# Kernel optimization log

Hardware: AMD Instinct MI355X
Metric: run time of the kernel (lower is better)

The kernel has to match this reference:

```python
import jax, jax.numpy as jnp
import numpy as np

N_NODES = 100000
N_EDGES = 2000000
FEAT = 4
H = 64
L = 3  # num_mp_layers
E = 2  # edge_types


def _p(key, shape, scale=0.05):
    return jax.random.normal(key, shape, dtype=jnp.float32) * scale


def setup_inputs() -> dict:
    key = jax.random.key(0)
    ks = jax.random.split(key, 24)
    inp = {
        "x": jax.random.normal(ks[0], (N_NODES, FEAT), dtype=jnp.float32),
        "node_type": jax.random.randint(ks[1], (N_NODES,), 0, 3),
        "edge_index": jax.random.randint(ks[2], (2, N_EDGES), 0, N_NODES),
        "edge_type": jax.random.randint(ks[3], (N_EDGES,), 0, E),
        # input_proj: Linear(4,64) + LayerNorm(64)
        "in_w": _p(ks[4], (FEAT, H)), "in_b": _p(ks[5], (H,)),
        "ln_g": jnp.ones((H,), jnp.float32), "ln_b": jnp.zeros((H,), jnp.float32),
        # per-layer, per-edge-type message MLPs: Linear(2H,H) -> ReLU -> Linear(H,H)
        "mlp_w1": _p(ks[6], (L, E, 2 * H, H)), "mlp_b1": _p(ks[7], (L, E, H)),
        "mlp_w2": _p(ks[8], (L, E, H, H)), "mlp_b2": _p(ks[9], (L, E, H)),
        # per-layer GRUCell(H,H): gates ordered [r, z, n] as in torch
        "gru_wi": _p(ks[10], (L, H, 3 * H)), "gru_wh": _p(ks[11], (L, H, 3 * H)),
        "gru_bi": _p(ks[12], (L, 3 * H)), "gru_bh": _p(ks[13], (L, 3 * H)),
        # readout: Linear(H,H) -> ReLU -> Linear(H,1)
        "ro_w1": _p(ks[14], (H, H)), "ro_b1": _p(ks[15], (H,)),
        "ro_w2": _p(ks[16], (H, 1)), "ro_b2": _p(ks[17], (1,)),
    }
    return inp


def _layernorm(h, g, b, eps=1e-5):
    mu = jnp.mean(h, axis=-1, keepdims=True)
    var = jnp.mean(jnp.square(h - mu), axis=-1, keepdims=True)
    return (h - mu) * jax.lax.rsqrt(var + eps) * g + b


def _forward(x, edge_index, edge_type, node_type,
             in_w, in_b, ln_g, ln_b,
             mlp_w1, mlp_b1, mlp_w2, mlp_b2,
             gru_wi, gru_wh, gru_bi, gru_bh,
             ro_w1, ro_b1, ro_w2, ro_b2):
    n = x.shape[0]
    # input projection (dropout is identity at inference)
    h = jax.nn.relu(_layernorm(x @ in_w + in_b, ln_g, ln_b))
    src, dst = edge_index[0], edge_index[1]
    for l in range(L):
        # gather -> concat: (M, 2H)
        mi = jnp.concatenate([h[src], h[dst]], axis=1)
        msg = jnp.zeros((mi.shape[0], H), dtype=h.dtype)
        for e in range(E):
            m = jax.nn.relu(mi @ mlp_w1[l, e] + mlp_b1[l, e]) @ mlp_w2[l, e] + mlp_b2[l, e]
            msg = msg + jnp.where((edge_type == e)[:, None], m, jnp.zeros((), h.dtype))
        # scatter_add over destination nodes
        agg = jax.ops.segment_sum(msg, dst, num_segments=n)
        # GRUCell(agg, h), torch gate order [r, z, n]
        gi = agg @ gru_wi[l] + gru_bi[l]
        gh = h @ gru_wh[l] + gru_bh[l]
        i_r, i_z, i_n = jnp.split(gi, 3, axis=-1)
        h_r, h_z, h_n = jnp.split(gh, 3, axis=-1)
        r = jax.nn.sigmoid(i_r + h_r)
        z = jax.nn.sigmoid(i_z + h_z)
        nn_ = jnp.tanh(i_n + r * h_n)
        h = (1.0 - z) * nn_ + z * h
    out = jax.nn.relu(h @ ro_w1 + ro_b1) @ ro_w2 + ro_b2  # (N, 1)
    # additive correction for data qubits (node_type==0); other nodes zeroed
    corr = jnp.where(node_type == 0, x[:, 0] + out[:, 0], jnp.zeros((), x.dtype))
    return corr


def reference(x, node_type, edge_index, edge_type,
              in_w, in_b, ln_g, ln_b,
              mlp_w1, mlp_b1, mlp_w2, mlp_b2,
              gru_wi, gru_wh, gru_bi, gru_bh,
              ro_w1, ro_b1, ro_w2, ro_b2):
    return _forward(x, edge_index, edge_type, node_type,
                    in_w, in_b, ln_g, ln_b,
                    mlp_w1, mlp_b1, mlp_w2, mlp_b2,
                    gru_wi, gru_wh, gru_bi, gru_bh,
                    ro_w1, ro_b1, ro_w2, ro_b2)
```

## Files before the change

### kernel.cpp

```cpp
#include <hip/hip_runtime.h>

typedef unsigned int u32;
typedef unsigned short u16;
typedef unsigned long long u64;

using short8 = __attribute__((ext_vector_type(8))) short;
using f32x4  = __attribute__((ext_vector_type(4))) float;

__device__ __forceinline__ u32 f2bf(float f) {
    u32 u = __float_as_uint(f);
    return (u + 0x7fffu + ((u >> 16) & 1u)) >> 16;
}
__device__ __forceinline__ u32 pk(float a, float b) {
    return f2bf(a) | (f2bf(b) << 16);
}
__device__ __forceinline__ u32 f2bf_fast(float f) {
    return (__float_as_uint(f) + 0x8000u) >> 16;
}
__device__ __forceinline__ u32 pk_fast(float a, float b) {
    return f2bf_fast(a) | (f2bf_fast(b) << 16);
}
__device__ __forceinline__ float bflo(u32 u) { return __uint_as_float(u << 16); }
__device__ __forceinline__ float bfhi(u32 u) { return __uint_as_float(u & 0xffff0000u); }
__device__ __forceinline__ float bfu(u16 u) { return __uint_as_float(((u32)u) << 16); }

union U8 { u32 u[4]; short8 v; };

__global__ void k_input_proj(const float* __restrict__ x, const float* __restrict__ in_w,
                             const float* __restrict__ in_b, const float* __restrict__ ln_g,
                             const float* __restrict__ ln_b, u16* __restrict__ hbf,
                             float* __restrict__ agg, int n_nodes) {
    const int lane = threadIdx.x & 63;
    const int node = blockIdx.x * 4 + (threadIdx.x >> 6);
    if (node >= n_nodes) return;
    agg[(size_t)node * 64 + lane] = 0.f;
    float acc = in_b[lane];
#pragma unroll
    for (int k = 0; k < 4; ++k) acc = fmaf(x[node * 4 + k], in_w[k * 64 + lane], acc);
    float s = acc;
#pragma unroll
    for (int off = 32; off > 0; off >>= 1) s += __shfl_xor(s, off);
    float mu = s * (1.f / 64.f);
    float d = acc - mu;
    float vs = d * d;
#pragma unroll
    for (int off = 32; off > 0; off >>= 1) vs += __shfl_xor(vs, off);
    float inv = rsqrtf(vs * (1.f / 64.f) + 1e-5f);
    float hv = fmaxf(d * inv * ln_g[lane] + ln_b[lane], 0.f);
    hbf[(size_t)node * 64 + lane] = (u16)f2bf(hv);
}

__global__ void k_hist(const int* __restrict__ dst, const int* __restrict__ ety,
                       int* __restrict__ cnt, int* __restrict__ key, int M, int N) {
    int i = blockIdx.x * 256 + threadIdx.x;
    if (i < M) {
        int k = (ety[i] & 1) * N + dst[i];
        key[i] = k;
        atomicAdd(&cnt[k], 1);
    }
}

__global__ void k_scan1(int* __restrict__ data, int* __restrict__ part, int N) {
    __shared__ int s[1024];
    const int t = threadIdx.x;
    const int i = blockIdx.x * 1024 + t;
    int v = (i < N) ? data[i] : 0;
    s[t] = v;
    __syncthreads();
#pragma unroll
    for (int d = 1; d < 1024; d <<= 1) {
        int x = (t >= d) ? s[t - d] : 0;
        __syncthreads();
        s[t] += x;
        __syncthreads();
    }
    if (i < N) data[i] = s[t] - v;
    if (t == 1023) part[blockIdx.x] = s[1023];
}

__global__ void k_scan2(int* __restrict__ part, int nb) {
    const int l = threadIdx.x & 63;
    int base = 0;
    for (int s = 0; s < nb; s += 64) {
        int i = s + l;
        int orig = (i < nb) ? part[i] : 0;
        int x = orig;
#pragma unroll
        for (int off = 1; off < 64; off <<= 1) {
            int t = __shfl_up(x, off);
            if (l >= off) x += t;
        }
        if (i < nb) part[i] = base + x - orig;
        base += __shfl(x, 63);
    }
}

__global__ void k_scan3(int* __restrict__ data, const int* __restrict__ part, int N,
                        int saveIdx, int* __restrict__ slot) {
    int i = blockIdx.x * 1024 + threadIdx.x;
    if (i < N) {
        int v = data[i] + part[blockIdx.x];
        data[i] = v;
        if (i == saveIdx) slot[0] = v;
    }
}

__global__ void k_filldst(const int* __restrict__ off, int* __restrict__ dstP,
                          int NB, int N, int M) {
    int b = blockIdx.x * 256 + threadIdx.x;
    if (b >= NB) return;
    int s = off[b];
    int e = (b + 1 < NB) ? off[b + 1] : M;
    int d = (b >= N) ? b - N : b;
    for (int p = s; p < e; ++p) dstP[p] = d;
}

__global__ void k_scatter(const int* __restrict__ src, const int* __restrict__ key,
                          int* __restrict__ cursor, int* __restrict__ srcP,
                          int M, int N, int nd8) {
    const int g = blockIdx.x & 7;
    const int nb = gridDim.x >> 3;
    const int bi = blockIdx.x >> 3;
    for (int e = bi * 256 + threadIdx.x; e < M; e += nb * 256) {
        int k = key[e];
        int d = (k >= N) ? k - N : k;
        if (d / nd8 == g) {
            int pos = atomicAdd(&cursor[k], 1);
            srcP[pos] = src[e] & 0x3FFFFFFF;
        }
    }
}

__global__ __launch_bounds__(256, 2) void k_edge_mlp(
    const u16* __restrict__ hbf, const int* __restrict__ srcP, const int* __restrict__ dstP,
    const int* __restrict__ t0p, const float* __restrict__ w1, const float* __restrict__ b1,
    const float* __restrict__ w2, const float* __restrict__ b2,
    float* __restrict__ agg, int M) {
    __shared__ u16 sHid[4][4608];
    __shared__ u16 sMsg[4][4864];

    const int tid = threadIdx.x;
    const int l = tid & 63, wv = tid >> 6;
    const int l15 = l & 15, quad = l >> 4;
    const f32x4 vz = {0.f, 0.f, 0.f, 0.f};

    const int T0 = *t0p;
    const int half = gridDim.x >> 1;
    const int ty = (blockIdx.x >= half) ? 1 : 0;
    const int bi = ty ? (int)blockIdx.x - half : (int)blockIdx.x;

    const int n_tiles = (M + 63) >> 6;
    const int tlo = ty ? (T0 >> 6) : 0;
    const int thi = ty ? n_tiles : ((T0 + 63) >> 6);
    const int lo = ty ? T0 : 0;
    const int hi = ty ? M : T0;
    const int range = thi - tlo;
    const int per = (range + half - 1) / half;
    const int c0 = tlo + bi * per;
    const int c1 = min(c0 + per, thi);

    short8 Bf1[4][4], Bf2[2][4];
    float b1r[4], b2r[4];
#pragma unroll
    for (int ni = 0; ni < 4; ++ni) {
        const int c = ni * 16 + l15;
        b1r[ni] = b1[ty * 64 + c];
        b2r[ni] = b2[ty * 64 + c];
#pragma unroll
        for (int s = 0; s < 4; ++s) {
            U8 tmp;
            const float* wp = w1 + (size_t)ty * 8192 + (size_t)(s * 32 + quad * 8) * 64 + c;
#pragma unroll
            for (int jp = 0; jp < 4; ++jp) tmp.u[jp] = pk(wp[(2 * jp) * 64], wp[(2 * jp + 1) * 64]);
            Bf1[s][ni] = tmp.v;
        }
#pragma unroll
        for (int s = 0; s < 2; ++s) {
            U8 tmp;
            const float* wp = w2 + (size_t)ty * 4096 + (size_t)(s * 32 + quad * 8) * 64 + c;
#pragma unroll
            for (int jp = 0; jp < 4; ++jp) tmp.u[jp] = pk(wp[(2 * jp) * 64], wp[(2 * jp + 1) * 64]);
            Bf2[s][ni] = tmp.v;
        }
    }

    u16* hid = sHid[wv];
    u16* msg = sMsg[wv];

    int t = c0 + wv;
    int mdc = -1;
    int msn = 0, mdn = -1;
    short8 a1[4][4];
    if (t < c1) {
        int ec = min((t << 6) + l, M - 1);
        int ms = srcP[ec];
        mdc = dstP[ec];
#pragma unroll
        for (int mi = 0; mi < 4; ++mi) {
            int rs = __shfl(ms, mi * 16 + l15);
            int rd = __shfl(mdc, mi * 16 + l15);
#pragma unroll
            for (int s = 0; s < 4; ++s) {
                const int row = (s < 2) ? rs : rd;
                a1[mi][s] = *(const short8*)(hbf + (size_t)row * 64 + (s & 1) * 32 + quad * 8);
            }
        }
        int ecn = min(((t + 4) << 6) + l, M - 1);
        msn = srcP[ecn];
        mdn = dstP[ecn];
    }

    for (; t < c1; t += 4) {
        const int base = t << 6;
        const int ecf = min(((t + 8) << 6) + l, M - 1);
        const int msf = srcP[ecf];
        const int mdf = dstP[ecf];

#pragma unroll
        for (int mi = 0; mi < 4; ++mi) {
            f32x4 acc[4] = {vz, vz, vz, vz};
#pragma unroll
            for (int s = 0; s < 4; ++s)
#pragma unroll
                for (int ni = 0; ni < 4; ++ni)
                    acc[ni] = __builtin_amdgcn_mfma_f32_16x16x32_bf16(a1[mi][s], Bf1[s][ni], acc[ni], 0, 0, 0);
            {
                int rs = __shfl(msn, mi * 16 + l15);
                int rd = __shfl(mdn, mi * 16 + l15);
#pragma unroll
                for (int s = 0; s < 4; ++s) {
                    const int row = (s < 2) ? rs : rd;
                    a1[mi][s] = *(const short8*)(hbf + (size_t)row * 64 + (s & 1) * 32 + quad * 8);
                }
            }
#pragma unroll
            for (int ni = 0; ni < 4; ++ni) {
                const int c = ni * 16 + l15;
#pragma unroll
                for (int r = 0; r < 4; ++r) {
                    float hv = fmaxf(acc[ni][r] + b1r[ni], 0.f);
                    hid[(mi * 16 + quad * 4 + r) * 72 + c] = (u16)f2bf_fast(hv);
                }
            }
        }

#pragma unroll
        for (int mi = 0; mi < 4; ++mi) {
            short8 a2a = *(const short8*)(hid + (mi * 16 + l15) * 72 + quad * 8);
            short8 a2b = *(const short8*)(hid + (mi * 16 + l15) * 72 + 32 + quad * 8);
#pragma unroll
            for (int ni = 0; ni < 4; ++ni) {
                f32x4 tt = __builtin_amdgcn_mfma_f32_16x16x32_bf16(a2a, Bf2[0][ni], vz, 0, 0, 0);
                f32x4 m2 = __builtin_amdgcn_mfma_f32_16x16x32_bf16(a2b, Bf2[1][ni], tt, 0, 0, 0);
                const int c = ni * 16 + l15;
                const int e0 = mi * 16 + quad * 4;
                const float bb = b2r[ni];
                uint2 w;
                w.x = pk_fast(m2[0] + bb, m2[1] + bb);
                w.y = pk_fast(m2[2] + bb, m2[3] + bb);
                *(uint2*)(msg + c * 76 + e0) = w;
            }
        }

        {
            int eg = base + l;
            int dvz = (eg >= lo && eg < hi) ? mdc : -1;
            int dprev = __shfl_up(dvz, 1);
            u64 mask = __ballot((l == 0) || (dvz != dprev));
            float a = 0.f;
#pragma unroll
            for (int i = 0; i < 64; i += 4) {
                uint2 pr = *(const uint2*)(msg + l * 76 + i);
                float v0 = bflo(pr.x), v1 = bfhi(pr.x), v2 = bflo(pr.y), v3 = bfhi(pr.y);
#define RR_STEP(ii, vv)                                                         \
                a += (vv);                                                      \
                if ((ii) == 63 || ((mask >> ((ii) + 1)) & 1ull)) {              \
                    int dd = __builtin_amdgcn_readlane(dvz, (ii));              \
                    if (dd >= 0) unsafeAtomicAdd(agg + (size_t)dd * 64 + l, a); \
                    a = 0.f;                                                    \
                }
                RR_STEP(i, v0)
                RR_STEP(i + 1, v1)
                RR_STEP(i + 2, v2)
                RR_STEP(i + 3, v3)
#undef RR_STEP
            }
        }
        mdc = mdn;
        msn = msf;
        mdn = mdf;
    }
}

__global__ __launch_bounds__(256, 2) void k_gru_gemm(
    float* __restrict__ agg, u16* __restrict__ hbf,
    const float* __restrict__ wi, const float* __restrict__ wh,
    const float* __restrict__ bi, const float* __restrict__ bh, int n_nodes, int last,
    const float* __restrict__ ro_w1, const float* __restrict__ ro_b1,
    const float* __restrict__ ro_w2, const float* __restrict__ ro_b2,
    const float* __restrict__ x, const int* __restrict__ node_type, float* __restrict__ out) {
    extern __shared__ u16 smem[];
    u16* sRZ = smem;
    u16* sIN = smem + 128 * 136;
    u16* sHN = sIN + 64 * 72;
    u16* sTR = sHN + 64 * 72;
    u16* sRO = sTR + 4 * 16 * 72;

    const int tid = threadIdx.x;
    const int l = tid & 63, wv = tid >> 6;
    const int l15 = l & 15, quad = l >> 4;
    const f32x4 vz = {0.f, 0.f, 0.f, 0.f};

    for (int u = tid; u < 128 * 64; u += 256) {
        int c = u & 127, k0 = (u >> 7) * 2;
        float v0 = (k0 < 64) ? wi[k0 * 192 + c] : wh[(k0 - 64) * 192 + c];
        float v1 = (k0 < 64) ? wi[(k0 + 1) * 192 + c] : wh[(k0 + 1 - 64) * 192 + c];
        *(u32*)(sRZ + c * 136 + k0) = pk(v0, v1);
    }
    for (int u = tid; u < 64 * 32; u += 256) {
        int c = u & 63, k0 = (u >> 6) * 2;
        *(u32*)(sIN + c * 72 + k0) = pk(wi[k0 * 192 + 128 + c], wi[(k0 + 1) * 192 + 128 + c]);
        *(u32*)(sHN + c * 72 + k0) = pk(wh[k0 * 192 + 128 + c], wh[(k0 + 1) * 192 + 128 + c]);
        *(u32*)(sRO + c * 72 + k0) = pk(ro_w1[k0 * 64 + c], ro_w1[(k0 + 1) * 64 + c]);
    }
    float bR[4], bZ[4], bI[4], bH[4], b1v[4], w2v[4];
#pragma unroll
    for (int nt = 0; nt < 4; ++nt) {
        int j = nt * 16 + l15;
        bR[nt] = bi[j] + bh[j];
        bZ[nt] = bi[64 + j] + bh[64 + j];
        bI[nt] = bi[128 + j];
        bH[nt] = bh[128 + j];
        b1v[nt] = ro_b1[j];
        w2v[nt] = ro_w2[j];
    }
    const float b2s = ro_b2[0];
    __syncthreads();

    u16* tr = sTR + wv * (16 * 72);
    const f32x4 z4 = {0.f, 0.f, 0.f, 0.f};
    const int n_tiles = (n_nodes + 15) >> 4;
    const int g = blockIdx.x & 7, jb = blockIdx.x >> 3, nbg = gridDim.x >> 3;
    const int per8 = (n_tiles + 7) >> 3;
    const int glo = g * per8, ghi = min(glo + per8, n_tiles);
    for (int tile = glo + jb * 4 + wv; tile < ghi; tile += nbg * 4) {
        const int nb = tile << 4;
        const int arow = nb + l15;
        const int rowc = (arow < n_nodes) ? arow : (n_nodes - 1);
        short8 aA[2], aH[2];
#pragma unroll
        for (int s = 0; s < 2; ++s) {
            const float* ap = agg + (size_t)rowc * 64 + s * 32 + quad * 8;
            U8 tt;
#pragma unroll
            for (int jp = 0; jp < 4; ++jp) tt.u[jp] = pk(ap[2 * jp], ap[2 * jp + 1]);
            aA[s] = tt.v;
            aH[s] = *(const short8*)(hbf + (size_t)rowc * 64 + s * 32 + quad * 8);
        }
        if (!last && arow < n_nodes) {
#pragma unroll
            for (int s = 0; s < 2; ++s) {
                *(f32x4*)(agg + (size_t)rowc * 64 + s * 32 + quad * 8) = z4;
                *(f32x4*)(agg + (size_t)rowc * 64 + s * 32 + quad * 8 + 4) = z4;
            }
        }
        f32x4 D[16];
#pragma unroll
        for (int i = 0; i < 16; ++i) D[i] = vz;
#pragma unroll
        for (int nt = 0; nt < 8; ++nt) {
            const u16* bp = sRZ + (nt * 16 + l15) * 136 + quad * 8;
            D[nt] = __builtin_amdgcn_mfma_f32_16x16x32_bf16(aA[0], *(const short8*)bp, D[nt], 0, 0, 0);
            D[nt] = __builtin_amdgcn_mfma_f32_16x16x32_bf16(aA[1], *(const short8*)(bp + 32), D[nt], 0, 0, 0);
            D[nt] = __builtin_amdgcn_mfma_f32_16x16x32_bf16(aH[0], *(const short8*)(bp + 64), D[nt], 0, 0, 0);
            D[nt] = __builtin_amdgcn_mfma_f32_16x16x32_bf16(aH[1], *(const short8*)(bp + 96), D[nt], 0, 0, 0);
        }
#pragma unroll
        for (int nt = 0; nt < 4; ++nt) {
            const u16* ip = sIN + (nt * 16 + l15) * 72 + quad * 8;
            D[8 + nt] = __builtin_amdgcn_mfma_f32_16x16x32_bf16(aA[0], *(const short8*)ip, D[8 + nt], 0, 0, 0);
            D[8 + nt] = __builtin_amdgcn_mfma_f32_16x16x32_bf16(aA[1], *(const short8*)(ip + 32), D[8 + nt], 0, 0, 0);
            const u16* hp = sHN + (nt * 16 + l15) * 72 + quad * 8;
            D[12 + nt] = __builtin_amdgcn_mfma_f32_16x16x32_bf16(aH[0], *(const short8*)hp, D[12 + nt], 0, 0, 0);
            D[12 + nt] = __builtin_amdgcn_mfma_f32_16x16x32_bf16(aH[1], *(const short8*)(hp + 32), D[12 + nt], 0, 0, 0);
        }
#pragma unroll
        for (int nt = 0; nt < 4; ++nt) {
            const int j = nt * 16 + l15;
#pragma unroll
            for (int r = 0; r < 4; ++r) {
                const int nd = nb + quad * 4 + r;
                float rsv = D[nt][r] + bR[nt];
                float zsv = D[4 + nt][r] + bZ[nt];
                float inv = D[8 + nt][r] + bI[nt];
                float hnv = D[12 + nt][r] + bH[nt];
                float rr = 1.f / (1.f + __expf(-rsv));
                float zz = 1.f / (1.f + __expf(-zsv));
                float nn = tanhf(fmaf(rr, hnv, inv));
                float hv = (nd < n_nodes) ? bfu(hbf[(size_t)nd * 64 + j]) : 0.f;
                float nh = (1.f - zz) * nn + zz * hv;
                tr[(quad * 4 + r) * 72 + j] = (u16)f2bf(nh);
            }
        }
        {
            const int nd = nb + (l >> 2);
            if (nd < n_nodes) {
                const u16* sp = tr + (l >> 2) * 72 + (l & 3) * 16;
                uint4 va = *(const uint4*)sp;
                uint4 vb = *(const uint4*)(sp + 8);
                u16* dp = hbf + (size_t)nd * 64 + (l & 3) * 16;
                *(uint4*)dp = va;
                *(uint4*)(dp + 8) = vb;
            }
        }
        if (last) {
            short8 ar0 = *(const short8*)(tr + l15 * 72 + quad * 8);
            short8 ar1 = *(const short8*)(tr + l15 * 72 + 32 + quad * 8);
            float p[4] = {0.f, 0.f, 0.f, 0.f};
#pragma unroll
            for (int nt = 0; nt < 4; ++nt) {
                const u16* bp = sRO + (nt * 16 + l15) * 72 + quad * 8;
                f32x4 acc = __builtin_amdgcn_mfma_f32_16x16x32_bf16(ar0, *(const short8*)bp, vz, 0, 0, 0);
                acc = __builtin_amdgcn_mfma_f32_16x16x32_bf16(ar1, *(const short8*)(bp + 32), acc, 0, 0, 0);
#pragma unroll
                for (int r = 0; r < 4; ++r)
                    p[r] += fmaxf(acc[r] + b1v[nt], 0.f) * w2v[nt];
            }
#pragma unroll
            for (int off = 1; off < 16; off <<= 1)
#pragma unroll
                for (int r = 0; r < 4; ++r) p[r] += __shfl_xor(p[r], off);
            if (l15 == 0) {
#pragma unroll
                for (int r = 0; r < 4; ++r) {
                    const int nd = nb + quad * 4 + r;
                    if (nd < n_nodes) {
                        float o = p[r] + b2s;
                        out[nd] = (node_type[nd] == 0) ? (x[nd * 4] + o) : 0.f;
                    }
                }
            }
        }
    }
}

extern "C" void kernel_launch(void* const* d_in, const int* in_sizes, int n_in, void* d_out,
                              int out_size, void* d_ws, size_t ws_size, hipStream_t stream) {
    const float* x = (const float*)d_in[0];
    const int* node_type = (const int*)d_in[1];
    const int* edge_index = (const int*)d_in[2];
    const int* edge_type = (const int*)d_in[3];
    const float* in_w = (const float*)d_in[4];
    const float* in_b = (const float*)d_in[5];
    const float* ln_g = (const float*)d_in[6];
    const float* ln_b = (const float*)d_in[7];
    const float* mlp_w1 = (const float*)d_in[8];
    const float* mlp_b1 = (const float*)d_in[9];
    const float* mlp_w2 = (const float*)d_in[10];
    const float* mlp_b2 = (const float*)d_in[11];
    const float* gru_wi = (const float*)d_in[12];
    const float* gru_wh = (const float*)d_in[13];
    const float* gru_bi = (const float*)d_in[14];
    const float* gru_bh = (const float*)d_in[15];
    const float* ro_w1 = (const float*)d_in[16];
    const float* ro_b1 = (const float*)d_in[17];
    const float* ro_w2 = (const float*)d_in[18];
    const float* ro_b2 = (const float*)d_in[19];

    const int N = in_sizes[1];
    const int M = in_sizes[3];
    const int* src = edge_index;
    const int* dst = edge_index + M;

    char* wsb = (char*)d_ws;
    float* agg = (float*)wsb;
    u16* hbf = (u16*)(wsb + (size_t)N * 256);
    int* off = (int*)(wsb + (size_t)N * 384);
    int* part = (int*)(wsb + (size_t)N * 384 + (size_t)2 * N * 4);
    int* srcP = (int*)(wsb + (size_t)N * 384 + (size_t)2 * N * 4 + 4096);
    int* dstP = srcP + M;
    int* key = dstP + M;
    int* t0slot = part + 1000;

    const int NB = 2 * N;
    const int nb = (NB + 1023) / 1024;
    const int nd8 = (N + 7) / 8;

    hipMemsetAsync(off, 0, (size_t)NB * sizeof(int), stream);
    k_hist<<<(M + 255) / 256, 256, 0, stream>>>(dst, edge_type, off, key, M, N);
    k_scan1<<<nb, 1024, 0, stream>>>(off, part, NB);
    k_scan2<<<1, 64, 0, stream>>>(part, nb);
    k_scan3<<<nb, 1024, 0, stream>>>(off, part, NB, N, t0slot);
    k_filldst<<<(NB + 255) / 256, 256, 0, stream>>>(off, dstP, NB, N, M);
    k_scatter<<<2048, 256, 0, stream>>>(src, key, off, srcP, M, N, nd8);

    k_input_proj<<<(N + 3) / 4, 256, 0, stream>>>(x, in_w, in_b, ln_g, ln_b, hbf, agg, N);
    const size_t gruLds =
        (size_t)(128 * 136 + 64 * 72 + 64 * 72 + 4 * 16 * 72 + 64 * 72) * sizeof(u16);
    for (int l = 0; l < 3; ++l) {
        k_edge_mlp<<<1024, 256, 0, stream>>>(hbf, srcP, dstP, t0slot,
                                             mlp_w1 + (size_t)l * 2 * 128 * 64,
                                             mlp_b1 + (size_t)l * 2 * 64,
                                             mlp_w2 + (size_t)l * 2 * 64 * 64,
                                             mlp_b2 + (size_t)l * 2 * 64, agg, M);
        k_gru_gemm<<<1024, 256, gruLds, stream>>>(agg, hbf, gru_wi + (size_t)l * 64 * 192,
                                                  gru_wh + (size_t)l * 64 * 192,
                                                  gru_bi + (size_t)l * 192, gru_bh + (size_t)l * 192,
                                                  N, (l == 2) ? 1 : 0,
                                                  ro_w1, ro_b1, ro_w2, ro_b2,
                                                  x, node_type, (float*)d_out);
    }
}
```

Baseline: 741.9 us.

## Keep edge-MLP hidden activations in registers by transposing first MFMA

Swaps the operand order of the first-layer MFMA so the output is transposed, with each lane holding hidden features along K for its edge column. The first-layer output then packs directly into bf16 A-operand fragments for the second-layer MFMA. This removes the shared-memory hidden buffer and its store/load round trip, and reorders the w2 fragment rows and b1 bias layout to match. It cuts LDS traffic and LDS footprint, which may allow more occupancy, but it depends on the register fragment mapping being exactly right.

```diff
diff --git a/kernel.cpp b/kernel.cpp
--- a/kernel.cpp
+++ b/kernel.cpp
@@ -136,7 +136,6 @@
     const int* __restrict__ t0p, const float* __restrict__ w1, const float* __restrict__ b1,
     const float* __restrict__ w2, const float* __restrict__ b2,
     float* __restrict__ agg, int M) {
-    __shared__ u16 sHid[4][4608];
     __shared__ u16 sMsg[4][4864];
 
     const int tid = threadIdx.x;
@@ -160,12 +159,13 @@
     const int c1 = min(c0 + per, thi);
 
     short8 Bf1[4][4], Bf2[2][4];
-    float b1r[4], b2r[4];
+    float b1p[4][4], b2r[4];
 #pragma unroll
     for (int ni = 0; ni < 4; ++ni) {
         const int c = ni * 16 + l15;
-        b1r[ni] = b1[ty * 64 + c];
         b2r[ni] = b2[ty * 64 + c];
+#pragma unroll
+        for (int r = 0; r < 4; ++r) b1p[ni][r] = b1[ty * 64 + ni * 16 + quad * 4 + r];
 #pragma unroll
         for (int s = 0; s < 4; ++s) {
             U8 tmp;
@@ -177,14 +177,16 @@
 #pragma unroll
         for (int s = 0; s < 2; ++s) {
             U8 tmp;
-            const float* wp = w2 + (size_t)ty * 4096 + (size_t)(s * 32 + quad * 8) * 64 + c;
-#pragma unroll
-            for (int jp = 0; jp < 4; ++jp) tmp.u[jp] = pk(wp[(2 * jp) * 64], wp[(2 * jp + 1) * 64]);
+#pragma unroll
+            for (int w = 0; w < 4; ++w) {
+                const int row = s * 32 + (w >> 1) * 16 + quad * 4 + (w & 1) * 2;
+                const float* wp = w2 + (size_t)ty * 4096 + (size_t)row * 64 + c;
+                tmp.u[w] = pk(wp[0], wp[64]);
+            }
             Bf2[s][ni] = tmp.v;
         }
     }
 
-    u16* hid = sHid[wv];
     u16* msg = sMsg[wv];
 
     int t = c0 + wv;
@@ -223,7 +225,7 @@
             for (int s = 0; s < 4; ++s)
 #pragma unroll
                 for (int ni = 0; ni < 4; ++ni)
-                    acc[ni] = __builtin_amdgcn_mfma_f32_16x16x32_bf16(a1[mi][s], Bf1[s][ni], acc[ni], 0, 0, 0);
+                    acc[ni] = __builtin_amdgcn_mfma_f32_16x16x32_bf16(Bf1[s][ni], a1[mi][s], acc[ni], 0, 0, 0);
             {
                 int rs = __shfl(msn, mi * 16 + l15);
                 int rd = __shfl(mdn, mi * 16 + l15);
@@ -233,25 +235,29 @@
                     a1[mi][s] = *(const short8*)(hbf + (size_t)row * 64 + (s & 1) * 32 + quad * 8);
                 }
             }
+            U8 pa, pb;
+#pragma unroll
+            for (int ni = 0; ni < 2; ++ni) {
+                float h0 = fmaxf(acc[ni][0] + b1p[ni][0], 0.f);
+                float h1 = fmaxf(acc[ni][1] + b1p[ni][1], 0.f);
+                float h2 = fmaxf(acc[ni][2] + b1p[ni][2], 0.f);
+                float h3 = fmaxf(acc[ni][3] + b1p[ni][3], 0.f);
+                pa.u[ni * 2] = pk_fast(h0, h1);
+                pa.u[ni * 2 + 1] = pk_fast(h2, h3);
+            }
+#pragma unroll
+            for (int ni = 0; ni < 2; ++ni) {
+                float h0 = fmaxf(acc[2 + ni][0] + b1p[2 + ni][0], 0.f);
+                float h1 = fmaxf(acc[2 + ni][1] + b1p[2 + ni][1], 0.f);
+                float h2 = fmaxf(acc[2 + ni][2] + b1p[2 + ni][2], 0.f);
+                float h3 = fmaxf(acc[2 + ni][3] + b1p[2 + ni][3], 0.f);
+                pb.u[ni * 2] = pk_fast(h0, h1);
+                pb.u[ni * 2 + 1] = pk_fast(h2, h3);
+            }
 #pragma unroll
             for (int ni = 0; ni < 4; ++ni) {
-                const int c = ni * 16 + l15;
-#pragma unroll
-                for (int r = 0; r < 4; ++r) {
-                    float hv = fmaxf(acc[ni][r] + b1r[ni], 0.f);
-                    hid[(mi * 16 + quad * 4 + r) * 72 + c] = (u16)f2bf_fast(hv);
-                }
-            }
-        }
-
-#pragma unroll
-        for (int mi = 0; mi < 4; ++mi) {
-            short8 a2a = *(const short8*)(hid + (mi * 16 + l15) * 72 + quad * 8);
-            short8 a2b = *(const short8*)(hid + (mi * 16 + l15) * 72 + 32 + quad * 8);
-#pragma unroll
-            for (int ni = 0; ni < 4; ++ni) {
-                f32x4 tt = __builtin_amdgcn_mfma_f32_16x16x32_bf16(a2a, Bf2[0][ni], vz, 0, 0, 0);
-                f32x4 m2 = __builtin_amdgcn_mfma_f32_16x16x32_bf16(a2b, Bf2[1][ni], tt, 0, 0, 0);
+                f32x4 tt = __builtin_amdgcn_mfma_f32_16x16x32_bf16(pa.v, Bf2[0][ni], vz, 0, 0, 0);
+                f32x4 m2 = __builtin_amdgcn_mfma_f32_16x16x32_bf16(pb.v, Bf2[1][ni], tt, 0, 0, 0);
                 const int c = ni * 16 + l15;
                 const int e0 = mi * 16 + quad * 4;
                 const float bb = b2r[ni];
```

Result: slower. 760.8 us (+2.5%).
